# Kernel optimization log

Measured on AMD Instinct MI355X. Metric: run time of the kernel, lower is better.

Reference implementation:

```python
import jax, jax.numpy as jnp
import numpy as np

EMB = 768          # MineModel.emb_size
HEADS = 4          # Mi hard-codes n_heads=4 for QTLayer
DK = EMB // HEADS  # 192
H_NEED = 3         # MineModel need_num_heads
QLEN = 10000
TLEN = 3000
EG = 100000        # give edges (before head replication)
EI = 100000        # inter_1 / inter_2 edges
NLAYERS = 2


def setup_inputs() -> dict:
    key = jax.random.key(0)
    ks = jax.random.split(key, 20)
    f = lambda k, s: jax.random.normal(k, s, dtype=jnp.float32) * 0.02
    return {
        'q_emb': jax.random.normal(ks[0], (QLEN, EMB), jnp.float32),
        't_emb': jax.random.normal(ks[1], (TLEN, EMB), jnp.float32),
        'give_src': jax.random.randint(ks[2], (EG,), 0, TLEN),
        'give_dst': jax.random.randint(ks[3], (EG,), 0, QLEN),
        'i1_src': jax.random.randint(ks[4], (EI,), 0, TLEN),
        'i1_dst': jax.random.randint(ks[5], (EI,), 0, TLEN),
        'i2_src': jax.random.randint(ks[6], (EI,), 0, TLEN),
        'i2_dst': jax.random.randint(ks[7], (EI,), 0, TLEN),
        'Wq_enc': f(ks[8], (EMB, EMB * H_NEED)),
        'bq_enc': jnp.zeros((EMB * H_NEED,), jnp.float32),
        'Wc': f(ks[9], (EMB, 10)),
        'bc': jnp.zeros((10,), jnp.float32),
        'centers': f(ks[10], (10, EMB)),
        'kW': f(ks[11], (NLAYERS, 2, EMB, EMB)),
        'kb': jnp.zeros((NLAYERS, 2, EMB), jnp.float32),
        'qW': f(ks[12], (NLAYERS, 2, EMB, EMB)),
        'qb': jnp.zeros((NLAYERS, 2, EMB), jnp.float32),
        'vW': f(ks[13], (NLAYERS, 2, EMB, EMB)),
        'vb': jnp.zeros((NLAYERS, 2, EMB), jnp.float32),
        'rel_att': f(ks[14], (NLAYERS, 3, HEADS, DK, DK)),
        'rel_msg': f(ks[15], (NLAYERS, 3, HEADS, DK, DK)),
        'rel_pri': jnp.ones((NLAYERS, 3, HEADS), jnp.float32),
        'Wout': f(ks[16], (EMB, EMB)),
        'bout': jnp.zeros((EMB,), jnp.float32),
    }


def _edge_softmax(score, dst, n_dst):
    # softmax over incoming edges of each destination node, per head
    m = jax.ops.segment_max(score, dst, num_segments=n_dst)      # [N, H]
    e = jnp.exp(score - m[dst])
    s = jax.ops.segment_sum(e, dst, num_segments=n_dst)
    return e / s[dst]


def _rel(k_src, v_src, q_dst, src, dst, n_dst, ratt, rmsg, rpri):
    # HGT relation: relation-specific K/V transform, edge dot-attention, scatter-sum
    k = jnp.einsum('nhd,hde->nhe', k_src, ratt)                  # [Nsrc, H, DK]
    v = jnp.einsum('nhd,hde->nhe', v_src, rmsg)
    score = jnp.einsum('ehd,ehd->eh', q_dst[dst], k[src]) * rpri / jnp.sqrt(jnp.float32(DK))
    a = _edge_softmax(score, dst, n_dst)                         # [E, H]
    return jax.ops.segment_sum(v[src] * a[:, :, None], dst, num_segments=n_dst)


def reference(q_emb, t_emb, give_src, give_dst, i1_src, i1_dst, i2_src, i2_dst,
              Wq_enc, bq_enc, Wc, bc, centers, kW, kb, qW, qb, vW, vb,
              rel_att, rel_msg, rel_pri, Wout, bout):
    n_q = QLEN * H_NEED
    # replicate 'give' edges per model-level head (cached graph construction)
    g_src = jnp.tile(give_src, H_NEED)
    g_dst = jnp.concatenate([give_dst + QLEN * i for i in range(H_NEED)])

    # question encoder -> split heads along feature dim, concat along rows
    q_hs = q_emb @ Wq_enc + bq_enc                               # [Q, EMB*H]
    q_h = q_hs.reshape(QLEN, H_NEED, EMB).transpose(1, 0, 2).reshape(n_q, EMB)
    q_h = q_h + jnp.tile(q_emb, (H_NEED, 1))
    assign = jax.nn.softmax(q_h @ Wc + bc, axis=-1)              # [n_q, 10]
    q_h = q_h + assign @ centers

    h_tag, h_q = t_emb, q_h
    for l in range(NLAYERS):
        k_tag = (h_tag @ kW[l, 0] + kb[l, 0]).reshape(-1, HEADS, DK)
        v_tag = (h_tag @ vW[l, 0] + vb[l, 0]).reshape(-1, HEADS, DK)
        q_tag = (h_tag @ qW[l, 0] + qb[l, 0]).reshape(-1, HEADS, DK)
        q_que = (h_q @ qW[l, 1] + qb[l, 1]).reshape(-1, HEADS, DK)
        t_q = _rel(k_tag, v_tag, q_que, g_src, g_dst, n_q,
                   rel_att[l, 0], rel_msg[l, 0], rel_pri[l, 0])
        t1 = _rel(k_tag, v_tag, q_tag, i1_src, i1_dst, TLEN,
                  rel_att[l, 1], rel_msg[l, 1], rel_pri[l, 1])
        t2 = _rel(k_tag, v_tag, q_tag, i2_src, i2_dst, TLEN,
                  rel_att[l, 2], rel_msg[l, 2], rel_pri[l, 2])
        # cross_reducer='mean' over the two tag->tag relations; residual add
        h_tag = (0.5 * (t1 + t2)).reshape(-1, EMB) + h_tag
        h_q = t_q.reshape(-1, EMB) + h_q

    ques_heads = h_q @ Wout + bout                               # [H*Q, EMB]
    tags = h_tag @ Wout + bout                                   # [T, EMB]
    # torch.split(.., q_len, dim=0) + stack(dim=1) -> [Q, H, EMB]
    ques = ques_heads.reshape(H_NEED, QLEN, EMB).transpose(1, 0, 2)
    return ques, tags
```

## Files before the change

### kernel.cpp

```cpp
#include <hip/hip_runtime.h>

#define QLEN 10000
#define TLEN 3000
#define EMB 768
#define HNEED 3
#define NQ (QLEN * HNEED)
#define EG 100000
#define EI 100000
#define DKH 192
#define NHEADS 4

namespace {

typedef unsigned short u16;
typedef unsigned char u8;
typedef unsigned int u32;
typedef __attribute__((ext_vector_type(8))) short bf16x8;
typedef __attribute__((ext_vector_type(4))) float f32x4;
typedef __attribute__((ext_vector_type(2))) float f32x2;

constexpr float SCALE = 0.07216878364870322f;

__device__ inline u16 f2bf(float f) {
  unsigned u = __float_as_uint(f);
  unsigned r = (u + 0x7FFFu + ((u >> 16) & 1u)) >> 16;
  return (u16)r;
}
__device__ inline float bf2f(u16 h) {
  return __uint_as_float((unsigned)h << 16);
}
__device__ inline u8 f2fp8(float f) {
  u32 pk = __builtin_amdgcn_cvt_pk_fp8_f32(f, f, 0, false);
  return (u8)(pk & 0xFF);
}
__device__ inline void decode12(const u32* p, float* o) {
#pragma unroll
  for (int t = 0; t < 3; ++t) {
    u32 w = p[t];
    f32x2 lo = __builtin_amdgcn_cvt_pk_f32_fp8(w, false);
    f32x2 hi = __builtin_amdgcn_cvt_pk_f32_fp8(w, true);
    o[t * 4 + 0] = lo[0]; o[t * 4 + 1] = lo[1];
    o[t * 4 + 2] = hi[0]; o[t * 4 + 3] = hi[1];
  }
}
__device__ inline f32x2 bfx2(u32 w) {
  f32x2 r;
  r[0] = __uint_as_float(w << 16);
  r[1] = __uint_as_float(w & 0xFFFF0000u);
  return r;
}

__device__ inline void gload_lds16(const u16* g, u16* s) {
  __builtin_amdgcn_global_load_lds(
      (const __attribute__((address_space(1))) unsigned*)g,
      (__attribute__((address_space(3))) unsigned*)s, 16, 0, 0);
}

template <int EPI, int OUT>
__global__ __launch_bounds__(256) void gemm_bf16(
    const u16* __restrict__ A, int lda, long long sAz,
    const u16* __restrict__ Bt, int ldb, long long sBz,
    void* __restrict__ Cv, int ldc, long long sCz, long long sCz2, int relpack,
    const float* __restrict__ bias, const u16* __restrict__ extra,
    int M, int N, int K)
{
  __shared__ __align__(16) u16 As[3][4096];
  __shared__ __align__(16) u16 Bs[3][4096];
  const int z = blockIdx.z;
  float* Cf = (float*)Cv;
  u16* Ch = (u16*)Cv;
  u8* C8 = (u8*)Cv;
  if (relpack) {
    const int zr = z >> 3, zh = z & 7;
    A += (long long)zh * sAz;
    Bt += (long long)z * sBz;
    const long long co = (long long)zr * sCz2 + (long long)zh * sCz;
    Cf += co; Ch += co; C8 += co;
  } else {
    A += (long long)z * sAz;
    Bt += (long long)z * sBz;
    Cf += (long long)z * sCz;
    Ch += (long long)z * sCz;
    C8 += (long long)z * sCz;
  }
  const int gx = gridDim.x;
  const int nwg = gx * gridDim.y;
  const int orig = blockIdx.y * gx + blockIdx.x;
  const int qq = nwg >> 3, rr = nwg & 7;
  const int xc = orig & 7, ix = orig >> 3;
  const int swz = (xc < rr ? xc * (qq + 1) : rr * (qq + 1) + (xc - rr) * qq) + ix;
  const int by = swz / gx, bx = swz - by * gx;
  const int bm = by * 128, bn = bx * 128;

  const int tid = threadIdx.x;
  const int w = tid >> 6, l = tid & 63;
  const int wr = w >> 1, wc = w & 1;
  const int l16 = l & 15, lk = l >> 4;
  const int srow = tid >> 2;
  const int scol = (((tid & 3) ^ ((srow >> 1) & 3))) * 8;
  const int rchunk = (lk ^ ((l16 >> 1) & 3));

  int r0 = bm + srow;      if (r0 > M - 1) r0 = M - 1;
  int r1 = bm + srow + 64; if (r1 > M - 1) r1 = M - 1;
  int c0 = bn + srow;      if (c0 > N - 1) c0 = N - 1;
  int c1 = bn + srow + 64; if (c1 > N - 1) c1 = N - 1;
  const u16* pa0 = A + (long long)r0 * lda + scol;
  const u16* pa1 = A + (long long)r1 * lda + scol;
  const u16* pb0 = Bt + (long long)c0 * ldb + scol;
  const u16* pb1 = Bt + (long long)c1 * ldb + scol;

  int aoff[4], boff[4];
#pragma unroll
  for (int m = 0; m < 4; ++m) {
    aoff[m] = (wr * 64 + m * 16 + l16) * 32 + rchunk * 8;
    boff[m] = (wc * 64 + m * 16 + l16) * 32 + rchunk * 8;
  }

  f32x4 acc[4][4] = {};
  const int nt = K / 32;

  auto stage = [&](int buf, int k0) {
    gload_lds16(pa0 + k0, &As[buf][w * 512]);
    gload_lds16(pa1 + k0, &As[buf][w * 512 + 2048]);
    gload_lds16(pb0 + k0, &Bs[buf][w * 512]);
    gload_lds16(pb1 + k0, &Bs[buf][w * 512 + 2048]);
  };

  stage(0, 0);
  stage(1, 32);
  int cur = 0, sb = 2;
  for (int t = 0; t < nt; ++t) {
    if (t < nt - 1)
      asm volatile("s_waitcnt vmcnt(4)" ::: "memory");
    else
      asm volatile("s_waitcnt vmcnt(0)" ::: "memory");
    __builtin_amdgcn_s_barrier();
    __builtin_amdgcn_sched_barrier(0);
    if (t + 2 < nt) {
      stage(sb, (t + 2) * 32);
      if (++sb == 3) sb = 0;
    }
    bf16x8 af[4], bf[4];
#pragma unroll
    for (int m = 0; m < 4; ++m)
      af[m] = *(const bf16x8*)&As[cur][aoff[m]];
#pragma unroll
    for (int n = 0; n < 4; ++n)
      bf[n] = *(const bf16x8*)&Bs[cur][boff[n]];
    __builtin_amdgcn_s_setprio(1);
#pragma unroll
    for (int m = 0; m < 4; ++m)
#pragma unroll
      for (int n = 0; n < 4; ++n)
        acc[m][n] = __builtin_amdgcn_mfma_f32_16x16x32_bf16(af[m], bf[n], acc[m][n], 0, 0, 0);
    __builtin_amdgcn_s_setprio(0);
    if (++cur == 3) cur = 0;
  }

#pragma unroll
  for (int m = 0; m < 4; ++m) {
#pragma unroll
    for (int j = 0; j < 4; ++j) {
      int grow = bm + wr * 64 + m * 16 + lk * 4 + j;
      if (grow >= M) continue;
#pragma unroll
      for (int n = 0; n < 4; ++n) {
        int gcol = bn + wc * 64 + n * 16 + l16;
        if (gcol >= N) continue;
        float val = acc[m][n][j] + (bias ? bias[gcol] : 0.f);
        if (EPI == 0) {
          if (OUT == 0)
            Cf[(long long)grow * ldc + gcol] = val;
          else if (OUT == 1)
            Ch[(long long)grow * ldc + gcol] = f2bf(val);
          else
            C8[(long long)grow * ldc + gcol] = f2fp8(val);
        } else if (EPI == 1) {
          int h = gcol / EMB, c = gcol - h * EMB;
          Ch[((long long)h * QLEN + grow) * EMB + c] =
              f2bf(val + bf2f(extra[(long long)grow * EMB + c]));
        } else {
          if (grow < NQ) {
            int i2 = grow % QLEN, h = grow / QLEN;
            Cf[((long long)i2 * HNEED + h) * EMB + gcol] = val;
          } else {
            Cf[(long long)grow * EMB + gcol] = val;
          }
        }
      }
    }
  }
}

__global__ void f2bf_kernel(const float* __restrict__ in, u16* __restrict__ out, long long n)
{
  long long i = ((long long)blockIdx.x * 256 + threadIdx.x) * 4;
  if (i >= n) return;
  float4 v = *(const float4*)(in + i);
  ushort4 o;
  o.x = f2bf(v.x); o.y = f2bf(v.y); o.z = f2bf(v.z); o.w = f2bf(v.w);
  *(ushort4*)(out + i) = o;
}

struct T12 {
  const float* s[12];
  u16* d[12];
  int ld[12];
};

__global__ __launch_bounds__(256) void transpose768(T12 jobs)
{
  const int z = blockIdx.z;
  const float* in = jobs.s[z];
  const long long ld = jobs.ld[z];
  u16* out = jobs.d[z];
  __shared__ float t[32][33];
  const int c0 = blockIdx.x * 32, r0 = blockIdx.y * 32;
  const int tx = threadIdx.x & 31, ty = threadIdx.x >> 5;
#pragma unroll
  for (int i = 0; i < 32; i += 8)
    t[ty + i][tx] = in[(long long)(r0 + ty + i) * ld + c0 + tx];
  __syncthreads();
#pragma unroll
  for (int i = 0; i < 32; i += 8)
    out[(long long)(c0 + ty + i) * 768 + r0 + tx] = f2bf(t[tx][ty + i]);
}

__global__ __launch_bounds__(256) void transpose_rel(
    const float* __restrict__ att, const float* __restrict__ msg,
    u16* __restrict__ relWT)
{
  const int z = blockIdx.z;
  const int isMsg = z >= 24;
  const int zz = isMsg ? z - 24 : z;
  const int lr = zz >> 2, h = zz & 3;
  const long long RS = (long long)DKH * DKH;
  const float* in = (isMsg ? msg : att) + (long long)zz * RS;
  u16* out = relWT + (long long)(lr * 8 + isMsg * 4 + h) * RS;
  __shared__ float t[32][33];
  const int c0 = blockIdx.x * 32, r0 = blockIdx.y * 32;
  const int tx = threadIdx.x & 31, ty = threadIdx.x >> 5;
#pragma unroll
  for (int i = 0; i < 32; i += 8)
    t[ty + i][tx] = in[(long long)(r0 + ty + i) * DKH + c0 + tx];
  __syncthreads();
#pragma unroll
  for (int i = 0; i < 32; i += 8)
    out[(long long)(c0 + ty + i) * DKH + r0 + tx] = f2bf(t[tx][ty + i]);
}

__global__ void pack_misc(const float* __restrict__ Wc, const float* __restrict__ kb,
                          const float* __restrict__ vb, const float* __restrict__ qb,
                          float* __restrict__ WcT, float* __restrict__ b_kvq)
{
  int idx = blockIdx.x * 256 + threadIdx.x;
  if (idx < 7680) {
    int j = idx / EMB, d = idx - j * EMB;
    WcT[idx] = Wc[d * 10 + j];
  } else if (idx < 7680 + 2 * 2304) {
    int k = idx - 7680;
    int l = k / 2304, c = k - l * 2304;
    float v;
    if (c < 768) v = kb[(l * 2) * EMB + c];
    else if (c < 1536) v = vb[(l * 2) * EMB + c - 768];
    else v = qb[(l * 2) * EMB + c - 1536];
    b_kvq[k] = v;
  }
}

__global__ __launch_bounds__(512) void assign_center512(
    u16* __restrict__ qh_bf,
    const float* __restrict__ WcT, const float* __restrict__ bc,
    const float* __restrict__ centers)
{
  __shared__ float wc_s[7680];
  __shared__ float cen_s[7680];
  const int tid = threadIdx.x;
  for (int i = tid; i < 7680; i += 512) {
    wc_s[i] = WcT[i];
    cen_s[i] = centers[i];
  }
  __syncthreads();
  const int wave = tid >> 6, lane = tid & 63;
  const int row = blockIdx.x * 8 + wave;
  const long long base = (long long)row * EMB;
  float x[12];
#pragma unroll
  for (int i = 0; i < 12; ++i) x[i] = bf2f(qh_bf[base + lane + 64 * i]);
  float part[10] = {};
#pragma unroll
  for (int i = 0; i < 12; ++i) {
    const float v = x[i];
    const int d = lane + 64 * i;
#pragma unroll
    for (int j = 0; j < 10; ++j) part[j] = fmaf(v, wc_s[j * EMB + d], part[j]);
  }
#pragma unroll
  for (int j = 0; j < 10; ++j)
#pragma unroll
    for (int off = 32; off; off >>= 1) part[j] += __shfl_xor(part[j], off);
  float mx = -1e30f;
#pragma unroll
  for (int j = 0; j < 10; ++j) { part[j] += bc[j]; mx = fmaxf(mx, part[j]); }
  float s = 0.f;
#pragma unroll
  for (int j = 0; j < 10; ++j) { part[j] = __expf(part[j] - mx); s += part[j]; }
  const float inv = 1.f / s;
#pragma unroll
  for (int i = 0; i < 12; ++i) {
    const int d = lane + 64 * i;
    float acc = 0.f;
#pragma unroll
    for (int j = 0; j < 10; ++j) acc = fmaf(part[j], cen_s[j * EMB + d], acc);
    qh_bf[base + d] = f2bf(x[i] + acc * inv);
  }
}

__global__ void hist_all(const int* __restrict__ gd, const int* __restrict__ d1,
                         const int* __restrict__ d2, int* __restrict__ cnt)
{
  int e = blockIdx.x * 256 + threadIdx.x;
  if (e < EG) atomicAdd(&cnt[gd[e]], 1);
  else if (e < EG + EI) atomicAdd(&cnt[QLEN + d1[e - EG]], 1);
  else if (e < EG + 2 * EI) atomicAdd(&cnt[QLEN + TLEN + d2[e - EG - EI]], 1);
}

__global__ __launch_bounds__(1024) void scan3(
    const int* __restrict__ cnt_all, int* __restrict__ rp_g,
    int* __restrict__ rp_1, int* __restrict__ rp_2, int* __restrict__ cur_all)
{
  __shared__ int buf[1024];
  const int b = blockIdx.x;
  const int n = (b == 0) ? QLEN : TLEN;
  const int seg = (b == 0) ? 0 : (b == 1) ? QLEN : QLEN + TLEN;
  const int* cnt = cnt_all + seg;
  int* cur = cur_all + seg;
  int* rowptr = (b == 0) ? rp_g : (b == 1) ? rp_1 : rp_2;
  const int tid = threadIdx.x;
  const int chunk = (n + 1023) >> 10;
  const int base = tid * chunk;
  int s = 0;
  for (int i = 0; i < chunk; ++i) {
    int idx = base + i;
    if (idx < n) s += cnt[idx];
  }
  buf[tid] = s;
  __syncthreads();
  for (int off = 1; off < 1024; off <<= 1) {
    int v = (tid >= off) ? buf[tid - off] : 0;
    __syncthreads();
    buf[tid] += v;
    __syncthreads();
  }
  int run = (tid == 0) ? 0 : buf[tid - 1];
  for (int i = 0; i < chunk; ++i) {
    int idx = base + i;
    if (idx < n) {
      rowptr[idx] = run;
      cur[idx] = run;
      run += cnt[idx];
    }
  }
  if (tid == 1023) rowptr[n] = buf[1023];
}

__global__ void fill_all(const int* __restrict__ gs, const int* __restrict__ gd,
                         const int* __restrict__ s1, const int* __restrict__ d1,
                         const int* __restrict__ s2, const int* __restrict__ d2,
                         int* __restrict__ cur_all, int* __restrict__ adj_all)
{
  int e = blockIdx.x * 256 + threadIdx.x;
  if (e < EG) {
    int p = atomicAdd(&cur_all[gd[e]], 1);
    adj_all[p] = gs[e];
  } else if (e < EG + EI) {
    int p = atomicAdd(&cur_all[QLEN + d1[e - EG]], 1);
    adj_all[EG + p] = s1[e - EG];
  } else if (e < EG + 2 * EI) {
    int p = atomicAdd(&cur_all[QLEN + TLEN + d2[e - EG - EI]], 1);
    adj_all[EG + EI + p] = s2[e - EG - EI];
  }
}

__global__ __launch_bounds__(256) void gather_give(
    const u8* __restrict__ q, const u8* __restrict__ kv,
    const int* __restrict__ rowptr, const int* __restrict__ adj,
    const float* __restrict__ rpri, u16* __restrict__ hq_bf)
{
  const int d = (blockIdx.x * 256 + threadIdx.x) >> 6;
  const int lane = threadIdx.x & 63;
  if (d >= QLEN) return;
  const int rs = rowptr[d], re = rowptr[d + 1];
  if (rs == re) return;
  const int h = lane >> 4, sub = lane & 15;
  const int off = h * DKH + sub * 12;
  const float pri = rpri[h] * SCALE;

  float qv[3][12];
#pragma unroll
  for (int c = 0; c < 3; ++c)
    decode12((const u32*)(q + (size_t)(c * QLEN + d) * EMB + off), qv[c]);

  float S[3] = {0.f, 0.f, 0.f};
  float A[3][12] = {};

  auto edge = [&](int sn) {
    float kf[12], vf[12];
    decode12((const u32*)(kv + (size_t)sn * 1536 + off), kf);
    decode12((const u32*)(kv + (size_t)sn * 1536 + 768 + off), vf);
    float dt[3] = {0.f, 0.f, 0.f};
#pragma unroll
    for (int t = 0; t < 12; ++t) {
#pragma unroll
      for (int c = 0; c < 3; ++c) dt[c] = fmaf(qv[c][t], kf[t], dt[c]);
    }
#pragma unroll
    for (int c = 0; c < 3; ++c) {
#pragma unroll
      for (int o2 = 8; o2; o2 >>= 1) dt[c] += __shfl_xor(dt[c], o2);
      const float e = __expf(dt[c] * pri);
      S[c] += e;
#pragma unroll
      for (int t = 0; t < 12; ++t) A[c][t] = fmaf(e, vf[t], A[c][t]);
    }
  };
  int i = rs;
  for (; i + 1 < re; i += 2) { edge(adj[i]); edge(adj[i + 1]); }
  if (i < re) edge(adj[i]);

#pragma unroll
  for (int c = 0; c < 3; ++c) {
    const float inv = 1.f / S[c];
    u32* o = (u32*)(hq_bf + (size_t)(c * QLEN + d) * EMB + off);
#pragma unroll
    for (int t = 0; t < 6; ++t) {
      f32x2 r = bfx2(o[t]);
      r[0] += A[c][2 * t] * inv;
      r[1] += A[c][2 * t + 1] * inv;
      o[t] = (u32)f2bf(r[0]) | ((u32)f2bf(r[1]) << 16);
    }
  }
}

__global__ __launch_bounds__(256) void gather_inter(
    const u16* __restrict__ tag_kvq,
    const u8* __restrict__ kv1, const u8* __restrict__ kv2,
    const int* __restrict__ rp1, const int* __restrict__ adj1,
    const int* __restrict__ rp2, const int* __restrict__ adj2,
    const float* __restrict__ pri1, const float* __restrict__ pri2,
    u16* __restrict__ htag_bf)
{
  const int d = (blockIdx.x * 256 + threadIdx.x) >> 6;
  const int lane = threadIdx.x & 63;
  if (d >= TLEN) return;
  const int rs1 = rp1[d], re1 = rp1[d + 1];
  const int rs2 = rp2[d], re2 = rp2[d + 1];
  if (rs1 == re1 && rs2 == re2) return;
  const int h = lane >> 4, sub = lane & 15;
  const int off = h * DKH + sub * 12;
  float qv[12];
  {
    const u32* qp = (const u32*)(tag_kvq + (size_t)d * 2304 + 1536 + off);
#pragma unroll
    for (int t = 0; t < 6; ++t) {
      f32x2 r = bfx2(qp[t]);
      qv[2 * t] = r[0]; qv[2 * t + 1] = r[1];
    }
  }
  float R[12] = {};
#pragma unroll
  for (int rel = 0; rel < 2; ++rel) {
    const u8* kv = rel ? kv2 : kv1;
    const int rs = rel ? rs2 : rs1, re = rel ? re2 : re1;
    const int* adj = rel ? adj2 : adj1;
    if (rs == re) continue;
    const float pri = (rel ? pri2[h] : pri1[h]) * SCALE;
    float S = 0.f, A[12] = {};
    auto edge = [&](int sn) {
      float kf[12], vf[12];
      decode12((const u32*)(kv + (size_t)sn * 1536 + off), kf);
      decode12((const u32*)(kv + (size_t)sn * 1536 + 768 + off), vf);
      float dt = 0.f;
#pragma unroll
      for (int t = 0; t < 12; ++t) dt = fmaf(qv[t], kf[t], dt);
#pragma unroll
      for (int o2 = 8; o2; o2 >>= 1) dt += __shfl_xor(dt, o2);
      const float e = __expf(dt * pri);
      S += e;
#pragma unroll
      for (int t = 0; t < 12; ++t) A[t] = fmaf(e, vf[t], A[t]);
    };
    int i = rs;
    for (; i + 1 < re; i += 2) { edge(adj[i]); edge(adj[i + 1]); }
    if (i < re) edge(adj[i]);
    const float inv = 0.5f / S;
#pragma unroll
    for (int t = 0; t < 12; ++t) R[t] = fmaf(A[t], inv, R[t]);
  }
  u32* o = (u32*)(htag_bf + (size_t)d * EMB + off);
#pragma unroll
  for (int t = 0; t < 6; ++t) {
    f32x2 r = bfx2(o[t]);
    r[0] += R[2 * t];
    r[1] += R[2 * t + 1];
    o[t] = (u32)f2bf(r[0]) | ((u32)f2bf(r[1]) << 16);
  }
}

}

extern "C" void kernel_launch(void* const* d_in, const int* in_sizes, int n_in,
                              void* d_out, int out_size, void* d_ws, size_t ws_size,
                              hipStream_t stream)
{
  const float* q_emb   = (const float*)d_in[0];
  const float* t_emb   = (const float*)d_in[1];
  const int*   give_src = (const int*)d_in[2];
  const int*   give_dst = (const int*)d_in[3];
  const int*   i1_src  = (const int*)d_in[4];
  const int*   i1_dst  = (const int*)d_in[5];
  const int*   i2_src  = (const int*)d_in[6];
  const int*   i2_dst  = (const int*)d_in[7];
  const float* Wq_enc  = (const float*)d_in[8];
  const float* bq_enc  = (const float*)d_in[9];
  const float* Wc      = (const float*)d_in[10];
  const float* bc      = (const float*)d_in[11];
  const float* centers = (const float*)d_in[12];
  const float* kW      = (const float*)d_in[13];
  const float* kb      = (const float*)d_in[14];
  const float* qW      = (const float*)d_in[15];
  const float* qb      = (const float*)d_in[16];
  const float* vW      = (const float*)d_in[17];
  const float* vb      = (const float*)d_in[18];
  const float* rel_att = (const float*)d_in[19];
  const float* rel_msg = (const float*)d_in[20];
  const float* rel_pri = (const float*)d_in[21];
  const float* Wout    = (const float*)d_in[22];
  const float* bout    = (const float*)d_in[23];
  float* out = (float*)d_out;

  const long long WS = (long long)EMB * EMB;
  const long long RS = (long long)DKH * DKH;

  float* p = (float*)d_ws;
  auto take = [&](size_t n) { float* r = p; p += ((n + 3) & ~(size_t)3); return r; };
  u16* h_q_bf    = (u16*)take((size_t)NQ * EMB / 2);
  u16* h_tag_bf  = (u16*)take((size_t)TLEN * EMB / 2);
  u16* q_emb_bf  = (u16*)take((size_t)QLEN * EMB / 2);
  u16* tag_kvq   = (u16*)take((size_t)TLEN * 2304 / 2);
  u8* kv_all     = (u8*)take((size_t)3 * TLEN * 1536 / 4);
  u8* kv_g = kv_all;
  u8* kv_1 = kv_all + (size_t)TLEN * 1536;
  u8* kv_2 = kv_all + (size_t)2 * TLEN * 1536;
  u16* WqT   = (u16*)take((size_t)3 * WS / 2);
  u16* qWT   = (u16*)take((size_t)2 * WS / 2);
  u16* Wtag  = (u16*)take((size_t)2 * 3 * WS / 2);
  u16* WoutT = (u16*)take((size_t)WS / 2);
  u16* relWT = (u16*)take((size_t)48 * RS / 2);
  float* WcT   = take(7680);
  float* b_kvq = take(2 * 2304);
  int* rp_g  = (int*)take(QLEN + 1);
  int* rp_1  = (int*)take(TLEN + 1);
  int* rp_2  = (int*)take(TLEN + 1);
  int* cur_all = (int*)take(QLEN + 2 * TLEN);
  int* cnt_all = (int*)take(QLEN + 2 * TLEN);
  int* adj_all = (int*)take(EG + 2 * EI);
  int* adj_g = adj_all;
  int* adj_1 = adj_all + EG;
  int* adj_2 = adj_all + EG + EI;
  u8* q_que = (u8*)out;

  auto gemmb = [&](int EPI, int OUT, const u16* A, int lda, long long sAz,
                   const u16* Bt, int ldb, long long sBz,
                   void* C, int ldc, long long sCz, long long sCz2, int relpack,
                   const float* bias, const u16* extra,
                   int M, int N, int K, int batch) {
    dim3 grid((N + 127) / 128, (M + 127) / 128, batch);
    if (EPI == 0 && OUT == 1)
      gemm_bf16<0, 1><<<grid, 256, 0, stream>>>(A, lda, sAz, Bt, ldb, sBz, C, ldc, sCz, sCz2, relpack, bias, extra, M, N, K);
    else if (EPI == 0 && OUT == 2)
      gemm_bf16<0, 2><<<grid, 256, 0, stream>>>(A, lda, sAz, Bt, ldb, sBz, C, ldc, sCz, sCz2, relpack, bias, extra, M, N, K);
    else if (EPI == 1)
      gemm_bf16<1, 1><<<grid, 256, 0, stream>>>(A, lda, sAz, Bt, ldb, sBz, C, ldc, sCz, sCz2, relpack, bias, extra, M, N, K);
    else
      gemm_bf16<2, 0><<<grid, 256, 0, stream>>>(A, lda, sAz, Bt, ldb, sBz, C, ldc, sCz, sCz2, relpack, bias, extra, M, N, K);
  };

  hipMemsetAsync(cnt_all, 0, (size_t)(QLEN + 2 * TLEN) * sizeof(int), stream);
  hist_all<<<(EG + 2 * EI + 255) / 256, 256, 0, stream>>>(give_dst, i1_dst, i2_dst, cnt_all);
  scan3<<<3, 1024, 0, stream>>>(cnt_all, rp_g, rp_1, rp_2, cur_all);
  fill_all<<<(EG + 2 * EI + 255) / 256, 256, 0, stream>>>(
      give_src, give_dst, i1_src, i1_dst, i2_src, i2_dst, cur_all, adj_all);

  pack_misc<<<48, 256, 0, stream>>>(Wc, kb, vb, qb, WcT, b_kvq);
  {
    T12 jobs;
    for (int j = 0; j < 3; ++j) { jobs.s[j] = Wq_enc + j * 768; jobs.d[j] = WqT + (long long)j * WS; jobs.ld[j] = 2304; }
    jobs.s[3] = qW + 1 * WS; jobs.d[3] = qWT;           jobs.ld[3] = 768;
    jobs.s[4] = qW + 3 * WS; jobs.d[4] = qWT + WS;      jobs.ld[4] = 768;
    for (int l = 0; l < 2; ++l) {
      jobs.s[5 + l * 3] = kW + (l * 2) * WS; jobs.d[5 + l * 3] = Wtag + (long long)(l * 3 + 0) * WS; jobs.ld[5 + l * 3] = 768;
      jobs.s[6 + l * 3] = vW + (l * 2) * WS; jobs.d[6 + l * 3] = Wtag + (long long)(l * 3 + 1) * WS; jobs.ld[6 + l * 3] = 768;
      jobs.s[7 + l * 3] = qW + (l * 2) * WS; jobs.d[7 + l * 3] = Wtag + (long long)(l * 3 + 2) * WS; jobs.ld[7 + l * 3] = 768;
    }
    jobs.s[11] = Wout; jobs.d[11] = WoutT; jobs.ld[11] = 768;
    transpose768<<<dim3(24, 24, 12), 256, 0, stream>>>(jobs);
  }
  transpose_rel<<<dim3(6, 6, 48), 256, 0, stream>>>(rel_att, rel_msg, relWT);

  f2bf_kernel<<<(QLEN * EMB / 4 + 255) / 256, 256, 0, stream>>>(q_emb, q_emb_bf, (long long)QLEN * EMB);
  gemmb(1, 1, q_emb_bf, EMB, 0, WqT, EMB, 0, h_q_bf, EMB, 0, 0, 0, bq_enc, q_emb_bf,
        QLEN, EMB * HNEED, EMB, 1);
  assign_center512<<<NQ / 8, 512, 0, stream>>>(h_q_bf, WcT, bc, centers);
  f2bf_kernel<<<(TLEN * EMB / 4 + 255) / 256, 256, 0, stream>>>(t_emb, h_tag_bf, (long long)TLEN * EMB);

  const long long KVZ = (long long)TLEN * 1536;
  for (int l = 0; l < 2; ++l) {
    gemmb(0, 1, h_tag_bf, EMB, 0, Wtag + (long long)l * 3 * WS, EMB, 0,
          tag_kvq, 2304, 0, 0, 0, b_kvq + l * 2304, nullptr, TLEN, 2304, EMB, 1);
    gemmb(0, 2, h_q_bf, EMB, 0, qWT + (long long)l * WS, EMB, 0,
          q_que, EMB, 0, 0, 0, qb + (l * 2 + 1) * EMB, nullptr, NQ, EMB, EMB, 1);
    gemmb(0, 2, tag_kvq, 2304, 192, relWT + (long long)(l * 3) * 8 * RS, DKH, RS,
          kv_g, 1536, 192, KVZ, 1, nullptr, nullptr, TLEN, DKH, DKH, 24);
    gather_give<<<(QLEN * 64 + 255) / 256, 256, 0, stream>>>(
        q_que, kv_g, rp_g, adj_g, rel_pri + (l * 3 + 0) * NHEADS, h_q_bf);
    gather_inter<<<(TLEN * 64 + 255) / 256, 256, 0, stream>>>(
        tag_kvq, kv_1, kv_2, rp_1, adj_1, rp_2, adj_2,
        rel_pri + (l * 3 + 1) * NHEADS, rel_pri + (l * 3 + 2) * NHEADS,
        h_tag_bf);
  }

  gemmb(2, 0, h_q_bf, EMB, 0, WoutT, EMB, 0, out, EMB, 0, 0, 0, bout, nullptr,
        NQ + TLEN, EMB, EMB, 1);
}
```

Baseline: 807.9 us.

## Fold relation matrices into K/V weights and merge per-layer GEMMs and gathers

Precomputes combined weights W_k·rel_att and W_v·rel_msg (plus combined biases) once per call, so per-layer relation K/V come straight from one GEMM on h_tag. This removes the separate tag K/V GEMM and the batched relation GEMM. The remaining per-layer projections (tag Q, question Q, three relation K/V) are packed into a single grouped GEMM launch. The give and inter gather kernels are merged into one launch. The trade-off is more K-dimension work per relation (768 instead of 192) and extra weight-prep kernels.

Result: faster. 761.3 us (-5.8%).

```diff
diff --git a/kernel.cpp b/kernel.cpp
--- a/kernel.cpp
+++ b/kernel.cpp
@@ -20,6 +20,8 @@
 typedef __attribute__((ext_vector_type(2))) float f32x2;
 
 constexpr float SCALE = 0.07216878364870322f;
+constexpr long long WS = (long long)EMB * EMB;
+constexpr long long RS = (long long)DKH * DKH;
 
 __device__ inline u16 f2bf(float f) {
   unsigned u = __float_as_uint(f);
@@ -56,11 +58,11 @@
       (__attribute__((address_space(3))) unsigned*)s, 16, 0, 0);
 }
 
-template <int EPI, int OUT>
+template <int EPI, int OUT, int MODE>
 __global__ __launch_bounds__(256) void gemm_bf16(
     const u16* __restrict__ A, int lda, long long sAz,
     const u16* __restrict__ Bt, int ldb, long long sBz,
-    void* __restrict__ Cv, int ldc, long long sCz, long long sCz2, int relpack,
+    void* __restrict__ Cv, int ldc, long long sCz,
     const float* __restrict__ bias, const u16* __restrict__ extra,
     int M, int N, int K)
 {
@@ -70,12 +72,12 @@
   float* Cf = (float*)Cv;
   u16* Ch = (u16*)Cv;
   u8* C8 = (u8*)Cv;
-  if (relpack) {
-    const int zr = z >> 3, zh = z & 7;
-    A += (long long)zh * sAz;
-    Bt += (long long)z * sBz;
-    const long long co = (long long)zr * sCz2 + (long long)zh * sCz;
-    Cf += co; Ch += co; C8 += co;
+  if (MODE == 1) {
+    const int lr = z >> 3, kv = (z >> 2) & 1, h = z & 3;
+    const int l = lr >= 3;
+    A += (long long)z * RS;
+    Bt = (kv ? extra : Bt) + (long long)(l * 2) * WS + h * 192;
+    Ch = (u16*)Cv + (long long)lr * 1536 * 768 + (long long)(kv * 768 + h * 192) * 768;
   } else {
     A += (long long)z * sAz;
     Bt += (long long)z * sBz;
@@ -192,6 +194,127 @@
   }
 }
 
+struct PackJobs {
+  const u16* A[5];
+  const u16* Bt[5];
+  void* C[5];
+  const float* bias[5];
+  int M[5];
+  int nx[5];
+  int ldc[5];
+  int out[5];
+  int start[6];
+};
+
+__global__ __launch_bounds__(256) void gemm_pack(PackJobs Jb)
+{
+  const int nwg = Jb.start[5];
+  const int orig = blockIdx.x;
+  const int qq = nwg >> 3, rr = nwg & 7;
+  const int xc = orig & 7, ix = orig >> 3;
+  const int swz = (xc < rr ? xc * (qq + 1) : rr * (qq + 1) + (xc - rr) * qq) + ix;
+  int j = 0;
+  while (swz >= Jb.start[j + 1]) ++j;
+  const int local = swz - Jb.start[j];
+  const int nx = Jb.nx[j];
+  const int by = local / nx, bx = local - by * nx;
+  const int bm = by * 128, bn = bx * 128;
+  const int M = Jb.M[j];
+  const int ldc = Jb.ldc[j];
+  const int outk = Jb.out[j];
+  const u16* A = Jb.A[j];
+  const u16* Bt = Jb.Bt[j];
+  const float* bias = Jb.bias[j];
+  u16* Ch = (u16*)Jb.C[j];
+  u8* C8 = (u8*)Jb.C[j];
+
+  __shared__ __align__(16) u16 As[3][4096];
+  __shared__ __align__(16) u16 Bs[3][4096];
+
+  const int tid = threadIdx.x;
+  const int w = tid >> 6, l = tid & 63;
+  const int wr = w >> 1, wc = w & 1;
+  const int l16 = l & 15, lk = l >> 4;
+  const int srow = tid >> 2;
+  const int scol = (((tid & 3) ^ ((srow >> 1) & 3))) * 8;
+  const int rchunk = (lk ^ ((l16 >> 1) & 3));
+
+  int r0 = bm + srow;      if (r0 > M - 1) r0 = M - 1;
+  int r1 = bm + srow + 64; if (r1 > M - 1) r1 = M - 1;
+  const int c0 = bn + srow;
+  const int c1 = bn + srow + 64;
+  const u16* pa0 = A + (long long)r0 * 768 + scol;
+  const u16* pa1 = A + (long long)r1 * 768 + scol;
+  const u16* pb0 = Bt + (long long)c0 * 768 + scol;
+  const u16* pb1 = Bt + (long long)c1 * 768 + scol;
+
+  int aoff[4], boff[4];
+#pragma unroll
+  for (int m = 0; m < 4; ++m) {
+    aoff[m] = (wr * 64 + m * 16 + l16) * 32 + rchunk * 8;
+    boff[m] = (wc * 64 + m * 16 + l16) * 32 + rchunk * 8;
+  }
+
+  f32x4 acc[4][4] = {};
+  const int nt = 24;
+
+  auto stage = [&](int buf, int k0) {
+    gload_lds16(pa0 + k0, &As[buf][w * 512]);
+    gload_lds16(pa1 + k0, &As[buf][w * 512 + 2048]);
+    gload_lds16(pb0 + k0, &Bs[buf][w * 512]);
+    gload_lds16(pb1 + k0, &Bs[buf][w * 512 + 2048]);
+  };
+
+  stage(0, 0);
+  stage(1, 32);
+  int cur = 0, sb = 2;
+  for (int t = 0; t < nt; ++t) {
+    if (t < nt - 1)
+      asm volatile("s_waitcnt vmcnt(4)" ::: "memory");
+    else
+      asm volatile("s_waitcnt vmcnt(0)" ::: "memory");
+    __builtin_amdgcn_s_barrier();
+    __builtin_amdgcn_sched_barrier(0);
+    if (t + 2 < nt) {
+      stage(sb, (t + 2) * 32);
+      if (++sb == 3) sb = 0;
+    }
+    bf16x8 af[4], bf[4];
+#pragma unroll
+    for (int m = 0; m < 4; ++m)
+      af[m] = *(const bf16x8*)&As[cur][aoff[m]];
+#pragma unroll
+    for (int n = 0; n < 4; ++n)
+      bf[n] = *(const bf16x8*)&Bs[cur][boff[n]];
+    __builtin_amdgcn_s_setprio(1);
+#pragma unroll
+    for (int m = 0; m < 4; ++m)
+#pragma unroll
+      for (int n = 0; n < 4; ++n)
+        acc[m][n] = __builtin_amdgcn_mfma_f32_16x16x32_bf16(af[m], bf[n], acc[m][n], 0, 0, 0);
+    __builtin_amdgcn_s_setprio(0);
+    if (++cur == 3) cur = 0;
+  }
+
+#pragma unroll
+  for (int m = 0; m < 4; ++m) {
+#pragma unroll
+    for (int j2 = 0; j2 < 4; ++j2) {
+      int grow = bm + wr * 64 + m * 16 + lk * 4 + j2;
+      if (grow >= M) continue;
+#pragma unroll
+      for (int n = 0; n < 4; ++n) {
+        int gcol = bn + wc * 64 + n * 16 + l16;
+        float val = acc[m][n][j2] + bias[gcol];
+        if (outk == 1)
+          Ch[(long long)grow * ldc + gcol] = f2bf(val);
+        else
+          C8[(long long)grow * ldc + gcol] = f2fp8(val);
+      }
+    }
+  }
+}
+
 __global__ void f2bf_kernel(const float* __restrict__ in, u16* __restrict__ out, long long n)
 {
   long long i = ((long long)blockIdx.x * 256 + threadIdx.x) * 4;
@@ -234,7 +357,6 @@
   const int isMsg = z >= 24;
   const int zz = isMsg ? z - 24 : z;
   const int lr = zz >> 2, h = zz & 3;
-  const long long RS = (long long)DKH * DKH;
   const float* in = (isMsg ? msg : att) + (long long)zz * RS;
   u16* out = relWT + (long long)(lr * 8 + isMsg * 4 + h) * RS;
   __shared__ float t[32][33];
@@ -249,23 +371,29 @@
     out[(long long)(c0 + ty + i) * DKH + r0 + tx] = f2bf(t[tx][ty + i]);
 }
 
-__global__ void pack_misc(const float* __restrict__ Wc, const float* __restrict__ kb,
-                          const float* __restrict__ vb, const float* __restrict__ qb,
-                          float* __restrict__ WcT, float* __restrict__ b_kvq)
+__global__ void pack_wct(const float* __restrict__ Wc, float* __restrict__ WcT)
 {
   int idx = blockIdx.x * 256 + threadIdx.x;
-  if (idx < 7680) {
-    int j = idx / EMB, d = idx - j * EMB;
-    WcT[idx] = Wc[d * 10 + j];
-  } else if (idx < 7680 + 2 * 2304) {
-    int k = idx - 7680;
-    int l = k / 2304, c = k - l * 2304;
-    float v;
-    if (c < 768) v = kb[(l * 2) * EMB + c];
-    else if (c < 1536) v = vb[(l * 2) * EMB + c - 768];
-    else v = qb[(l * 2) * EMB + c - 1536];
-    b_kvq[k] = v;
-  }
+  if (idx >= 7680) return;
+  int j = idx / EMB, d = idx - j * EMB;
+  WcT[idx] = Wc[d * 10 + j];
+}
+
+__global__ void bcomb_kernel(const float* __restrict__ kb, const float* __restrict__ vb,
+                             const float* __restrict__ att, const float* __restrict__ msg,
+                             float* __restrict__ bcomb)
+{
+  int idx = blockIdx.x * 256 + threadIdx.x;
+  if (idx >= 6 * 1536) return;
+  int lr = idx / 1536, n = idx - lr * 1536;
+  int kv = n / 768, n2 = n - kv * 768;
+  int h = n2 / 192, j = n2 - h * 192;
+  int l = lr / 3;
+  const float* bsrc = (kv ? vb : kb) + (l * 2) * EMB + h * 192;
+  const float* rl = (kv ? msg : att) + ((long long)lr * 4 + h) * RS + j;
+  float s = 0.f;
+  for (int e = 0; e < 192; ++e) s = fmaf(bsrc[e], rl[(long long)e * 192], s);
+  bcomb[idx] = s;
 }
 
 __global__ __launch_bounds__(512) void assign_center512(
@@ -382,128 +510,121 @@
   }
 }
 
-__global__ __launch_bounds__(256) void gather_give(
-    const u8* __restrict__ q, const u8* __restrict__ kv,
-    const int* __restrict__ rowptr, const int* __restrict__ adj,
-    const float* __restrict__ rpri, u16* __restrict__ hq_bf)
-{
-  const int d = (blockIdx.x * 256 + threadIdx.x) >> 6;
-  const int lane = threadIdx.x & 63;
-  if (d >= QLEN) return;
-  const int rs = rowptr[d], re = rowptr[d + 1];
-  if (rs == re) return;
-  const int h = lane >> 4, sub = lane & 15;
-  const int off = h * DKH + sub * 12;
-  const float pri = rpri[h] * SCALE;
-
-  float qv[3][12];
-#pragma unroll
-  for (int c = 0; c < 3; ++c)
-    decode12((const u32*)(q + (size_t)(c * QLEN + d) * EMB + off), qv[c]);
-
-  float S[3] = {0.f, 0.f, 0.f};
-  float A[3][12] = {};
-
-  auto edge = [&](int sn) {
-    float kf[12], vf[12];
-    decode12((const u32*)(kv + (size_t)sn * 1536 + off), kf);
-    decode12((const u32*)(kv + (size_t)sn * 1536 + 768 + off), vf);
-    float dt[3] = {0.f, 0.f, 0.f};
-#pragma unroll
-    for (int t = 0; t < 12; ++t) {
-#pragma unroll
-      for (int c = 0; c < 3; ++c) dt[c] = fmaf(qv[c][t], kf[t], dt[c]);
-    }
-#pragma unroll
-    for (int c = 0; c < 3; ++c) {
-#pragma unroll
-      for (int o2 = 8; o2; o2 >>= 1) dt[c] += __shfl_xor(dt[c], o2);
-      const float e = __expf(dt[c] * pri);
-      S[c] += e;
-#pragma unroll
-      for (int t = 0; t < 12; ++t) A[c][t] = fmaf(e, vf[t], A[c][t]);
-    }
-  };
-  int i = rs;
-  for (; i + 1 < re; i += 2) { edge(adj[i]); edge(adj[i + 1]); }
-  if (i < re) edge(adj[i]);
-
-#pragma unroll
-  for (int c = 0; c < 3; ++c) {
-    const float inv = 1.f / S[c];
-    u32* o = (u32*)(hq_bf + (size_t)(c * QLEN + d) * EMB + off);
-#pragma unroll
-    for (int t = 0; t < 6; ++t) {
-      f32x2 r = bfx2(o[t]);
-      r[0] += A[c][2 * t] * inv;
-      r[1] += A[c][2 * t + 1] * inv;
-      o[t] = (u32)f2bf(r[0]) | ((u32)f2bf(r[1]) << 16);
-    }
-  }
-}
-
-__global__ __launch_bounds__(256) void gather_inter(
-    const u16* __restrict__ tag_kvq,
-    const u8* __restrict__ kv1, const u8* __restrict__ kv2,
+__global__ __launch_bounds__(256) void gather_all(
+    const u8* __restrict__ q, const u8* __restrict__ kv_g,
+    const int* __restrict__ rp_g, const int* __restrict__ adj_g,
+    const float* __restrict__ pri_g, u16* __restrict__ hq_bf,
+    const u16* __restrict__ q_tag, const u8* __restrict__ kv1,
+    const u8* __restrict__ kv2,
     const int* __restrict__ rp1, const int* __restrict__ adj1,
     const int* __restrict__ rp2, const int* __restrict__ adj2,
     const float* __restrict__ pri1, const float* __restrict__ pri2,
     u16* __restrict__ htag_bf)
 {
-  const int d = (blockIdx.x * 256 + threadIdx.x) >> 6;
+  const int wid = blockIdx.x * 4 + (threadIdx.x >> 6);
   const int lane = threadIdx.x & 63;
-  if (d >= TLEN) return;
-  const int rs1 = rp1[d], re1 = rp1[d + 1];
-  const int rs2 = rp2[d], re2 = rp2[d + 1];
-  if (rs1 == re1 && rs2 == re2) return;
   const int h = lane >> 4, sub = lane & 15;
   const int off = h * DKH + sub * 12;
-  float qv[12];
-  {
-    const u32* qp = (const u32*)(tag_kvq + (size_t)d * 2304 + 1536 + off);
-#pragma unroll
-    for (int t = 0; t < 6; ++t) {
-      f32x2 r = bfx2(qp[t]);
-      qv[2 * t] = r[0]; qv[2 * t + 1] = r[1];
-    }
-  }
-  float R[12] = {};
-#pragma unroll
-  for (int rel = 0; rel < 2; ++rel) {
-    const u8* kv = rel ? kv2 : kv1;
-    const int rs = rel ? rs2 : rs1, re = rel ? re2 : re1;
-    const int* adj = rel ? adj2 : adj1;
-    if (rs == re) continue;
-    const float pri = (rel ? pri2[h] : pri1[h]) * SCALE;
-    float S = 0.f, A[12] = {};
+
+  if (wid < QLEN) {
+    const int d = wid;
+    const int rs = rp_g[d], re = rp_g[d + 1];
+    if (rs == re) return;
+    const float pri = pri_g[h] * SCALE;
+    float qv[3][12];
+#pragma unroll
+    for (int c = 0; c < 3; ++c)
+      decode12((const u32*)(q + (size_t)(c * QLEN + d) * EMB + off), qv[c]);
+    float S[3] = {0.f, 0.f, 0.f};
+    float A[3][12] = {};
     auto edge = [&](int sn) {
       float kf[12], vf[12];
-      decode12((const u32*)(kv + (size_t)sn * 1536 + off), kf);
-      decode12((const u32*)(kv + (size_t)sn * 1536 + 768 + off), vf);
-      float dt = 0.f;
-#pragma unroll
-      for (int t = 0; t < 12; ++t) dt = fmaf(qv[t], kf[t], dt);
-#pragma unroll
-      for (int o2 = 8; o2; o2 >>= 1) dt += __shfl_xor(dt, o2);
-      const float e = __expf(dt * pri);
-      S += e;
-#pragma unroll
-      for (int t = 0; t < 12; ++t) A[t] = fmaf(e, vf[t], A[t]);
+      decode12((const u32*)(kv_g + (size_t)sn * 1536 + off), kf);
+      decode12((const u32*)(kv_g + (size_t)sn * 1536 + 768 + off), vf);
+      float dt[3] = {0.f, 0.f, 0.f};
+#pragma unroll
+      for (int t = 0; t < 12; ++t) {
+#pragma unroll
+        for (int c = 0; c < 3; ++c) dt[c] = fmaf(qv[c][t], kf[t], dt[c]);
+      }
+#pragma unroll
+      for (int c = 0; c < 3; ++c) {
+#pragma unroll
+        for (int o2 = 8; o2; o2 >>= 1) dt[c] += __shfl_xor(dt[c], o2);
+        const float e = __expf(dt[c] * pri);
+        S[c] += e;
+#pragma unroll
+        for (int t = 0; t < 12; ++t) A[c][t] = fmaf(e, vf[t], A[c][t]);
+      }
     };
     int i = rs;
-    for (; i + 1 < re; i += 2) { edge(adj[i]); edge(adj[i + 1]); }
-    if (i < re) edge(adj[i]);
-    const float inv = 0.5f / S;
-#pragma unroll
-    for (int t = 0; t < 12; ++t) R[t] = fmaf(A[t], inv, R[t]);
-  }
-  u32* o = (u32*)(htag_bf + (size_t)d * EMB + off);
-#pragma unroll
-  for (int t = 0; t < 6; ++t) {
-    f32x2 r = bfx2(o[t]);
-    r[0] += R[2 * t];
-    r[1] += R[2 * t + 1];
-    o[t] = (u32)f2bf(r[0]) | ((u32)f2bf(r[1]) << 16);
+    for (; i + 1 < re; i += 2) { edge(adj_g[i]); edge(adj_g[i + 1]); }
+    if (i < re) edge(adj_g[i]);
+#pragma unroll
+    for (int c = 0; c < 3; ++c) {
+      const float inv = 1.f / S[c];
+      u32* o = (u32*)(hq_bf + (size_t)(c * QLEN + d) * EMB + off);
+#pragma unroll
+      for (int t = 0; t < 6; ++t) {
+        f32x2 r = bfx2(o[t]);
+        r[0] += A[c][2 * t] * inv;
+        r[1] += A[c][2 * t + 1] * inv;
+        o[t] = (u32)f2bf(r[0]) | ((u32)f2bf(r[1]) << 16);
+      }
+    }
+  } else {
+    const int d = wid - QLEN;
+    if (d >= TLEN) return;
+    const int rs1 = rp1[d], re1 = rp1[d + 1];
+    const int rs2 = rp2[d], re2 = rp2[d + 1];
+    if (rs1 == re1 && rs2 == re2) return;
+    float qv[12];
+    {
+      const u32* qp = (const u32*)(q_tag + (size_t)d * EMB + off);
+#pragma unroll
+      for (int t = 0; t < 6; ++t) {
+        f32x2 r = bfx2(qp[t]);
+        qv[2 * t] = r[0]; qv[2 * t + 1] = r[1];
+      }
+    }
+    float R[12] = {};
+#pragma unroll
+    for (int rel = 0; rel < 2; ++rel) {
+      const u8* kv = rel ? kv2 : kv1;
+      const int rs = rel ? rs2 : rs1, re = rel ? re2 : re1;
+      const int* adj = rel ? adj2 : adj1;
+      if (rs == re) continue;
+      const float pri = (rel ? pri2[h] : pri1[h]) * SCALE;
+      float S = 0.f, A[12] = {};
+      auto edge = [&](int sn) {
+        float kf[12], vf[12];
+        decode12((const u32*)(kv + (size_t)sn * 1536 + off), kf);
+        decode12((const u32*)(kv + (size_t)sn * 1536 + 768 + off), vf);
+        float dt = 0.f;
+#pragma unroll
+        for (int t = 0; t < 12; ++t) dt = fmaf(qv[t], kf[t], dt);
+#pragma unroll
+        for (int o2 = 8; o2; o2 >>= 1) dt += __shfl_xor(dt, o2);
+        const float e = __expf(dt * pri);
+        S += e;
+#pragma unroll
+        for (int t = 0; t < 12; ++t) A[t] = fmaf(e, vf[t], A[t]);
+      };
+      int i = rs;
+      for (; i + 1 < re; i += 2) { edge(adj[i]); edge(adj[i + 1]); }
+      if (i < re) edge(adj[i]);
+      const float inv = 0.5f / S;
+#pragma unroll
+      for (int t = 0; t < 12; ++t) R[t] = fmaf(A[t], inv, R[t]);
+    }
+    u32* o = (u32*)(htag_bf + (size_t)d * EMB + off);
+#pragma unroll
+    for (int t = 0; t < 6; ++t) {
+      f32x2 r = bfx2(o[t]);
+      r[0] += R[2 * t];
+      r[1] += R[2 * t + 1];
+      o[t] = (u32)f2bf(r[0]) | ((u32)f2bf(r[1]) << 16);
+    }
   }
 }
 
@@ -539,26 +660,25 @@
   const float* bout    = (const float*)d_in[23];
   float* out = (float*)d_out;
 
-  const long long WS = (long long)EMB * EMB;
-  const long long RS = (long long)DKH * DKH;
-
   float* p = (float*)d_ws;
   auto take = [&](size_t n) { float* r = p; p += ((n + 3) & ~(size_t)3); return r; };
   u16* h_q_bf    = (u16*)take((size_t)NQ * EMB / 2);
   u16* h_tag_bf  = (u16*)take((size_t)TLEN * EMB / 2);
   u16* q_emb_bf  = (u16*)take((size_t)QLEN * EMB / 2);
-  u16* tag_kvq   = (u16*)take((size_t)TLEN * 2304 / 2);
+  u16* q_tag_bf  = (u16*)take((size_t)TLEN * EMB / 2);
   u8* kv_all     = (u8*)take((size_t)3 * TLEN * 1536 / 4);
   u8* kv_g = kv_all;
   u8* kv_1 = kv_all + (size_t)TLEN * 1536;
   u8* kv_2 = kv_all + (size_t)2 * TLEN * 1536;
   u16* WqT   = (u16*)take((size_t)3 * WS / 2);
-  u16* qWT   = (u16*)take((size_t)2 * WS / 2);
-  u16* Wtag  = (u16*)take((size_t)2 * 3 * WS / 2);
+  u16* qWT   = (u16*)take((size_t)4 * WS / 2);
   u16* WoutT = (u16*)take((size_t)WS / 2);
   u16* relWT = (u16*)take((size_t)48 * RS / 2);
+  u16* kWbf  = (u16*)take((size_t)4 * WS / 2);
+  u16* vWbf  = (u16*)take((size_t)4 * WS / 2);
+  u16* Wcomb = (u16*)take((size_t)6 * 1536 * 768 / 2);
+  float* bcomb = take(6 * 1536);
   float* WcT   = take(7680);
-  float* b_kvq = take(2 * 2304);
   int* rp_g  = (int*)take(QLEN + 1);
   int* rp_1  = (int*)take(TLEN + 1);
   int* rp_2  = (int*)take(TLEN + 1);
@@ -570,66 +690,64 @@
   int* adj_2 = adj_all + EG + EI;
   u8* q_que = (u8*)out;
 
-  auto gemmb = [&](int EPI, int OUT, const u16* A, int lda, long long sAz,
-                   const u16* Bt, int ldb, long long sBz,
-                   void* C, int ldc, long long sCz, long long sCz2, int relpack,
-                   const float* bias, const u16* extra,
-                   int M, int N, int K, int batch) {
-    dim3 grid((N + 127) / 128, (M + 127) / 128, batch);
-    if (EPI == 0 && OUT == 1)
-      gemm_bf16<0, 1><<<grid, 256, 0, stream>>>(A, lda, sAz, Bt, ldb, sBz, C, ldc, sCz, sCz2, relpack, bias, extra, M, N, K);
-    else if (EPI == 0 && OUT == 2)
-      gemm_bf16<0, 2><<<grid, 256, 0, stream>>>(A, lda, sAz, Bt, ldb, sBz, C, ldc, sCz, sCz2, relpack, bias, extra, M, N, K);
-    else if (EPI == 1)
-      gemm_bf16<1, 1><<<grid, 256, 0, stream>>>(A, lda, sAz, Bt, ldb, sBz, C, ldc, sCz, sCz2, relpack, bias, extra, M, N, K);
-    else
-      gemm_bf16<2, 0><<<grid, 256, 0, stream>>>(A, lda, sAz, Bt, ldb, sBz, C, ldc, sCz, sCz2, relpack, bias, extra, M, N, K);
-  };
-
   hipMemsetAsync(cnt_all, 0, (size_t)(QLEN + 2 * TLEN) * sizeof(int), stream);
   hist_all<<<(EG + 2 * EI + 255) / 256, 256, 0, stream>>>(give_dst, i1_dst, i2_dst, cnt_all);
   scan3<<<3, 1024, 0, stream>>>(cnt_all, rp_g, rp_1, rp_2, cur_all);
   fill_all<<<(EG + 2 * EI + 255) / 256, 256, 0, stream>>>(
       give_src, give_dst, i1_src, i1_dst, i2_src, i2_dst, cur_all, adj_all);
 
-  pack_misc<<<48, 256, 0, stream>>>(Wc, kb, vb, qb, WcT, b_kvq);
+  pack_wct<<<30, 256, 0, stream>>>(Wc, WcT);
   {
     T12 jobs;
     for (int j = 0; j < 3; ++j) { jobs.s[j] = Wq_enc + j * 768; jobs.d[j] = WqT + (long long)j * WS; jobs.ld[j] = 2304; }
-    jobs.s[3] = qW + 1 * WS; jobs.d[3] = qWT;           jobs.ld[3] = 768;
-    jobs.s[4] = qW + 3 * WS; jobs.d[4] = qWT + WS;      jobs.ld[4] = 768;
-    for (int l = 0; l < 2; ++l) {
-      jobs.s[5 + l * 3] = kW + (l * 2) * WS; jobs.d[5 + l * 3] = Wtag + (long long)(l * 3 + 0) * WS; jobs.ld[5 + l * 3] = 768;
-      jobs.s[6 + l * 3] = vW + (l * 2) * WS; jobs.d[6 + l * 3] = Wtag + (long long)(l * 3 + 1) * WS; jobs.ld[6 + l * 3] = 768;
-      jobs.s[7 + l * 3] = qW + (l * 2) * WS; jobs.d[7 + l * 3] = Wtag + (long long)(l * 3 + 2) * WS; jobs.ld[7 + l * 3] = 768;
-    }
-    jobs.s[11] = Wout; jobs.d[11] = WoutT; jobs.ld[11] = 768;
-    transpose768<<<dim3(24, 24, 12), 256, 0, stream>>>(jobs);
+    for (int s = 0; s < 4; ++s) { jobs.s[3 + s] = qW + (long long)s * WS; jobs.d[3 + s] = qWT + (long long)s * WS; jobs.ld[3 + s] = 768; }
+    jobs.s[7] = Wout; jobs.d[7] = WoutT; jobs.ld[7] = 768;
+    for (int j = 8; j < 12; ++j) { jobs.s[j] = Wout; jobs.d[j] = WoutT; jobs.ld[j] = 768; }
+    transpose768<<<dim3(24, 24, 8), 256, 0, stream>>>(jobs);
   }
   transpose_rel<<<dim3(6, 6, 48), 256, 0, stream>>>(rel_att, rel_msg, relWT);
+  f2bf_kernel<<<(int)((4 * WS / 4 + 255) / 256), 256, 0, stream>>>(kW, kWbf, 4 * WS);
+  f2bf_kernel<<<(int)((4 * WS / 4 + 255) / 256), 256, 0, stream>>>(vW, vWbf, 4 * WS);
+  gemm_bf16<0, 1, 1><<<dim3(6, 2, 48), 256, 0, stream>>>(
+      relWT, DKH, 0, kWbf, EMB, 0, Wcomb, EMB, 0, nullptr, vWbf, DKH, EMB, DKH);
+  bcomb_kernel<<<36, 256, 0, stream>>>(kb, vb, rel_att, rel_msg, bcomb);
 
   f2bf_kernel<<<(QLEN * EMB / 4 + 255) / 256, 256, 0, stream>>>(q_emb, q_emb_bf, (long long)QLEN * EMB);
-  gemmb(1, 1, q_emb_bf, EMB, 0, WqT, EMB, 0, h_q_bf, EMB, 0, 0, 0, bq_enc, q_emb_bf,
-        QLEN, EMB * HNEED, EMB, 1);
+  gemm_bf16<1, 1, 0><<<dim3(18, 79, 1), 256, 0, stream>>>(
+      q_emb_bf, EMB, 0, WqT, EMB, 0, h_q_bf, EMB, 0, bq_enc, q_emb_bf,
+      QLEN, EMB * HNEED, EMB);
   assign_center512<<<NQ / 8, 512, 0, stream>>>(h_q_bf, WcT, bc, centers);
   f2bf_kernel<<<(TLEN * EMB / 4 + 255) / 256, 256, 0, stream>>>(t_emb, h_tag_bf, (long long)TLEN * EMB);
 
-  const long long KVZ = (long long)TLEN * 1536;
   for (int l = 0; l < 2; ++l) {
-    gemmb(0, 1, h_tag_bf, EMB, 0, Wtag + (long long)l * 3 * WS, EMB, 0,
-          tag_kvq, 2304, 0, 0, 0, b_kvq + l * 2304, nullptr, TLEN, 2304, EMB, 1);
-    gemmb(0, 2, h_q_bf, EMB, 0, qWT + (long long)l * WS, EMB, 0,
-          q_que, EMB, 0, 0, 0, qb + (l * 2 + 1) * EMB, nullptr, NQ, EMB, EMB, 1);
-    gemmb(0, 2, tag_kvq, 2304, 192, relWT + (long long)(l * 3) * 8 * RS, DKH, RS,
-          kv_g, 1536, 192, KVZ, 1, nullptr, nullptr, TLEN, DKH, DKH, 24);
-    gather_give<<<(QLEN * 64 + 255) / 256, 256, 0, stream>>>(
-        q_que, kv_g, rp_g, adj_g, rel_pri + (l * 3 + 0) * NHEADS, h_q_bf);
-    gather_inter<<<(TLEN * 64 + 255) / 256, 256, 0, stream>>>(
-        tag_kvq, kv_1, kv_2, rp_1, adj_1, rp_2, adj_2,
+    PackJobs J;
+    J.A[0] = h_tag_bf; J.Bt[0] = qWT + (long long)(l * 2) * WS; J.C[0] = q_tag_bf;
+    J.bias[0] = qb + (l * 2) * EMB; J.M[0] = TLEN; J.nx[0] = 6; J.ldc[0] = 768; J.out[0] = 1;
+    J.A[1] = h_q_bf; J.Bt[1] = qWT + (long long)(l * 2 + 1) * WS; J.C[1] = q_que;
+    J.bias[1] = qb + (l * 2 + 1) * EMB; J.M[1] = NQ; J.nx[1] = 6; J.ldc[1] = 768; J.out[1] = 2;
+    for (int r = 0; r < 3; ++r) {
+      J.A[2 + r] = h_tag_bf;
+      J.Bt[2 + r] = Wcomb + (long long)(l * 3 + r) * 1536 * 768;
+      J.C[2 + r] = kv_all + (size_t)r * TLEN * 1536;
+      J.bias[2 + r] = bcomb + (l * 3 + r) * 1536;
+      J.M[2 + r] = TLEN; J.nx[2 + r] = 12; J.ldc[2 + r] = 1536; J.out[2 + r] = 2;
+    }
+    J.start[0] = 0;
+    J.start[1] = 144;
+    J.start[2] = 144 + 1410;
+    J.start[3] = 1554 + 288;
+    J.start[4] = 1842 + 288;
+    J.start[5] = 2130 + 288;
+    gemm_pack<<<2418, 256, 0, stream>>>(J);
+
+    gather_all<<<(QLEN + TLEN) / 4 + 1, 256, 0, stream>>>(
+        q_que, kv_g, rp_g, adj_g, rel_pri + (l * 3 + 0) * NHEADS, h_q_bf,
+        q_tag_bf, kv_1, kv_2, rp_1, adj_1, rp_2, adj_2,
         rel_pri + (l * 3 + 1) * NHEADS, rel_pri + (l * 3 + 2) * NHEADS,
         h_tag_bf);
   }
 
-  gemmb(2, 0, h_q_bf, EMB, 0, WoutT, EMB, 0, out, EMB, 0, 0, 0, bout, nullptr,
-        NQ + TLEN, EMB, EMB, 1);
-}
+  gemm_bf16<2, 0, 0><<<dim3(6, 258, 1), 256, 0, stream>>>(
+      h_q_bf, EMB, 0, WoutT, EMB, 0, out, EMB, 0, bout, nullptr,
+      NQ + TLEN, EMB, EMB);
+}
```
